# Kernel tuning notes

Hardware: AMD Instinct MI355X
Metric: run time of the kernel (lower is better)

## Reference

```python
import jax, jax.numpy as jnp
from jax import lax
import numpy as np

GAMMA = 0.25        # inv_temp
C_SCALE = 1.0       # spectral_scale
STRIDE = 8          # patch stride (== patch_size, non-overlapping)


def setup_inputs() -> dict:
    key = jax.random.key(0)
    ks = jax.random.split(key, 9)
    B, C, H = 1024, 3, 64
    D, NP, M, NH, R, P = 256, 64, 1024, 8, 32, 8
    return {
        "x": jax.random.normal(ks[0], (B, C, H, H), jnp.float32),
        "z": jax.random.normal(ks[1], (B, NP, D), jnp.float32),
        "encoder_weight": jax.random.normal(ks[2], (D, C, P, P), jnp.float32) * 0.05,
        "encoder_bias": jax.random.normal(ks[3], (D,), jnp.float32) * 0.05,
        "visible_bias": jax.random.normal(ks[4], (C, H, H), jnp.float32) * 0.05,
        "pos_bias": jax.random.normal(ks[5], (NP, D), jnp.float32) * 0.05,
        "memory_weight": jax.random.normal(ks[6], (D, M), jnp.float32) * 0.05,
        "W_Q": jax.random.normal(ks[7], (NH, R, D), jnp.float32) * 0.05,
        "W_K": jax.random.normal(ks[8], (NH, R, D), jnp.float32) * 0.05,
    }


def reference(x, z, encoder_weight, encoder_bias, visible_bias, pos_bias,
              memory_weight, W_Q, W_K):
    """E = 0.5||x||^2 + 0.5||z||^2 - Phi_coupling(x, z); returns (B,)."""
    B = x.shape[0]
    D = encoder_weight.shape[0]

    quad_x = 0.5 * jnp.sum(x * x, axis=(1, 2, 3))
    quad_z = 0.5 * jnp.sum(z * z, axis=(1, 2))

    # visible-bias coupling
    phi_vis = jnp.sum(visible_bias[None] * x, axis=(1, 2, 3))

    # conv encode: (B, D, gh, gw) -> (B, NP, D)
    enc = lax.conv_general_dilated(
        x, C_SCALE * encoder_weight, window_strides=(STRIDE, STRIDE),
        padding='VALID', dimension_numbers=('NCHW', 'OIHW', 'NCHW'))
    encoded = enc.reshape(B, D, -1).transpose(0, 2, 1)  # (B, NP, D)

    # enc_act = 'none' -> identity
    phi_enc = jnp.sum(encoded * z, axis=(1, 2))
    phi_bias = jnp.sum(z * encoder_bias, axis=(1, 2))
    phi_pos = jnp.sum(z * pos_bias[None], axis=(1, 2))

    # memory ReLU^2 term: (B, NP, M)
    mem_proj = jnp.einsum('bpd,dm->bpm', z, C_SCALE * memory_weight)
    phi_mem = jnp.sum(jnp.square(jax.nn.relu(mem_proj)), axis=(1, 2))

    # Hopfield attention logsumexp term
    Q = jnp.einsum('bpd,hrd->bhrp', z, C_SCALE * W_Q)  # (B, H, R, NP)
    K = jnp.einsum('bpd,hrd->bhrp', z, C_SCALE * W_K)
    A = jnp.einsum('bhdm,bhdn->bhmn', Q, K)            # (B, H, NP, NP)
    phi_att = jnp.sum(jax.scipy.special.logsumexp(GAMMA * A, axis=-1),
                      axis=(1, 2)) / GAMMA

    coupling = phi_vis + phi_enc + phi_bias + phi_pos + phi_mem + phi_att
    return quad_x + quad_z - coupling
```

## Files before the change

kernel.cpp:

```cpp
#include <hip/hip_runtime.h>
#include <hip/hip_bf16.h>

#define GAMMA 0.25f


typedef __attribute__((ext_vector_type(8))) short short8;
typedef __attribute__((ext_vector_type(4))) float f32x4;

__device__ __forceinline__ float dot4(float4 a, float4 b) {
  return fmaf(a.x, b.x, fmaf(a.y, b.y, fmaf(a.z, b.z, a.w * b.w)));
}

__device__ __forceinline__ void fma4(float4& a, float s, float4 w) {
  a.x = fmaf(s, w.x, a.x); a.y = fmaf(s, w.y, a.y);
  a.z = fmaf(s, w.z, a.z); a.w = fmaf(s, w.w, a.w);
}

__device__ __forceinline__ ushort f2bf(float f) {
  __hip_bfloat16 h = __float2bfloat16(f);
  return *reinterpret_cast<ushort*>(&h);
}

__device__ __forceinline__ float bf2f(ushort u) {
  union { unsigned int i; float f; } v;
  v.i = ((unsigned int)u) << 16;
  return v.f;
}

__device__ __forceinline__ float block_sum_256(float v, float* tmp) {
#pragma unroll
  for (int off = 32; off; off >>= 1) v += __shfl_down(v, off, 64);
  int w = threadIdx.x >> 6;
  if ((threadIdx.x & 63) == 0) tmp[w] = v;
  __syncthreads();
  return tmp[0] + tmp[1] + tmp[2] + tmp[3];
}

__global__ __launch_bounds__(256) void k_z_cvt2(const float* __restrict__ z,
                                                const float* __restrict__ eb,
                                                const float* __restrict__ pb,
                                                float* __restrict__ out,
                                                ushort* __restrict__ zb16) {
  __shared__ float tmp[4];
  int bid = blockIdx.x, b = bid >> 1, hz = bid & 1, t = threadIdx.x;
  const float4* zb = (const float4*)(z + (size_t)b * 16384);
  const float4* pb4 = (const float4*)pb;
  const float4* eb4 = (const float4*)eb;
  ushort4* z16o = (ushort4*)(zb16 + (size_t)b * 16384);
  float s = 0.f;
  const int i0 = hz * 2048;
  for (int i = i0 + t; i < i0 + 2048; i += 256) {
    float4 zv = zb[i];
    float4 pv = pb4[i];
    float4 ev = eb4[i & 63];
    float4 c;
    c.x = pv.x + ev.x; c.y = pv.y + ev.y; c.z = pv.z + ev.z; c.w = pv.w + ev.w;
    s += 0.5f * dot4(zv, zv) - dot4(zv, c);
    ushort4 o;
    o.x = f2bf(zv.x); o.y = f2bf(zv.y); o.z = f2bf(zv.z); o.w = f2bf(zv.w);
    z16o[i] = o;
  }
  float r = block_sum_256(s, tmp);
  if (t == 0) atomicAdd(out + b, r);
}

__global__ __launch_bounds__(256) void k_cvt_weights_v4(
    const float* __restrict__ wq, const float* __restrict__ wk,
    const float* __restrict__ ew, const float* __restrict__ mw,
    ushort* __restrict__ wcf, ushort* __restrict__ ewt,
    ushort* __restrict__ mtf) {
  int bid = blockIdx.x, t = threadIdx.x;
  ushort o[8];
  if (bid < 64) {
    int tid = bid * 256 + t;
    int frag = tid >> 6, l = tid & 63;
    int ctg = frag >> 3, kc = frag & 7;
    int col = ctg * 16 + (l & 15);
    int h = col >> 6, qk = (col >> 5) & 1, rr = col & 31;
    int k0 = kc * 32 + (l >> 4) * 8;
    const float* s = (qk ? wk : wq) + ((size_t)h * 32 + rr) * 256 + k0;
#pragma unroll
    for (int i = 0; i < 8; ++i) o[i] = f2bf(s[i]);
    *(ushort4*)(wcf + (size_t)tid * 8) = *(ushort4*)&o[0];
    *(ushort4*)(wcf + (size_t)tid * 8 + 4) = *(ushort4*)&o[4];
  } else if (bid < 88) {
    int tid = (bid - 64) * 256 + t;
    int frag = tid >> 6, l = tid & 63;
    int ks = frag / 12, ct = frag % 12;
    const float* s = ew + (size_t)(ks * 32 + (l >> 4) * 8) * 192 +
                     ct * 16 + (l & 15);
#pragma unroll
    for (int i = 0; i < 8; ++i) o[i] = f2bf(s[(size_t)i * 192]);
    *(ushort4*)(ewt + (size_t)tid * 8) = *(ushort4*)&o[0];
    *(ushort4*)(ewt + (size_t)tid * 8 + 4) = *(ushort4*)&o[4];
  } else {
    int tid = (bid - 88) * 256 + t;
    int frag = tid >> 6, l = tid & 63;
    int C = frag >> 3, kc = frag & 7;
    int k0 = kc * 32 + (l >> 4) * 8, col = C * 16 + (l & 15);
#pragma unroll
    for (int i = 0; i < 8; ++i) o[i] = f2bf(mw[(size_t)(k0 + i) * 1024 + col]);
    *(ushort4*)(mtf + (size_t)tid * 8) = *(ushort4*)&o[0];
    *(ushort4*)(mtf + (size_t)tid * 8 + 4) = *(ushort4*)&o[4];
  }
}

__global__ __launch_bounds__(256) void k_enc_v4(
    const float* __restrict__ x, const float* __restrict__ vb,
    const ushort* __restrict__ ewt, const ushort* __restrict__ zb16,
    float* __restrict__ out) {
  __shared__ ushort xs[12288];
  __shared__ ushort ebuf[2][6144];
  __shared__ float tmp[4];
  const int b = blockIdx.x, t = threadIdx.x, l = t & 63, w = t >> 6;
  const int q = l >> 4, m = l & 15;

  const ushort* Az = zb16 + ((size_t)b * 64 + 16 * w + m) * 256 + q * 8;
  short8 a[8];
#pragma unroll
  for (int ks = 0; ks < 8; ++ks) a[ks] = *(const short8*)(Az + ks * 32);

  short8 st[3];
#pragma unroll
  for (int i = 0; i < 3; ++i)
    st[i] = *(const short8*)(ewt + (size_t)(t + i * 256) * 8);

  const float4* xb = (const float4*)(x + (size_t)b * 12288);
  const float4* vb4 = (const float4*)vb;
  ushort4* xs4 = (ushort4*)xs;
  float s = 0.f;
  for (int i = t; i < 3072; i += 256) {
    float4 xv = xb[i];
    float4 bv = vb4[i];
    s += 0.5f * dot4(xv, xv) - dot4(bv, xv);
    ushort4 o;
    o.x = f2bf(xv.x); o.y = f2bf(xv.y); o.z = f2bf(xv.z); o.w = f2bf(xv.w);
    xs4[i] = o;
  }
#pragma unroll
  for (int i = 0; i < 3; ++i)
    *(short8*)(ebuf[0] + (size_t)(t + i * 256) * 8) = st[i];
  __syncthreads();

  f32x4 acc[12];
#pragma unroll
  for (int ct = 0; ct < 12; ++ct) acc[ct] = f32x4{0.f, 0.f, 0.f, 0.f};

#pragma unroll
  for (int ks = 0; ks < 8; ++ks) {
    const int cur = ks & 1;
    if (ks < 7) {
#pragma unroll
      for (int i = 0; i < 3; ++i)
        st[i] = *(const short8*)(ewt + (size_t)(ks + 1) * 6144 +
                                 (size_t)(t + i * 256) * 8);
    }
#pragma unroll
    for (int ct = 0; ct < 12; ++ct) {
      short8 bv = *(const short8*)(ebuf[cur] + (size_t)(ct * 64 + l) * 8);
      acc[ct] = __builtin_amdgcn_mfma_f32_16x16x32_bf16(a[ks], bv, acc[ct], 0, 0, 0);
    }
    if (ks < 7) {
#pragma unroll
      for (int i = 0; i < 3; ++i)
        *(short8*)(ebuf[cur ^ 1] + (size_t)(t + i * 256) * 8) = st[i];
    }
    __syncthreads();
  }

#pragma unroll
  for (int ct = 0; ct < 12; ++ct) {
#pragma unroll
    for (int reg = 0; reg < 4; ++reg) {
      const int p = 16 * w + 4 * q + reg, gi = p >> 3, gj = p & 7;
      const int k = ct * 16 + m, c = k >> 6, r2 = k & 63;
      const int ii = r2 >> 3, jj = r2 & 7;
      s -= acc[ct][reg] * bf2f(xs[c * 4096 + (gi * 8 + ii) * 64 + gj * 8 + jj]);
    }
  }
  float r = block_sum_256(s, tmp);
  if (t == 0) atomicAdd(out + b, r);
}

__global__ __launch_bounds__(256) void k_mem_v5(const ushort* __restrict__ zb,
                                                const ushort* __restrict__ mtf,
                                                float* __restrict__ out) {
  __shared__ ushort zf[2048 * 8];
  __shared__ float tmp[4];
  const int t = threadIdx.x, l = t & 63, w = t >> 6;
  const int b = blockIdx.x >> 1, cth = blockIdx.x & 1;

#pragma unroll
  for (int j = 0; j < 8; ++j) {
    int i = t + j * 256;
    int l2 = i & 63, ks = (i >> 6) & 7, w2 = i >> 9;
    short8 v = *(const short8*)(zb + ((size_t)b * 64 + 16 * w2 + (l2 & 15)) * 256
                                + ks * 32 + (l2 >> 4) * 8);
    *(short8*)(zf + (size_t)i * 8) = v;
  }
  __syncthreads();

  float s = 0.f;
#pragma unroll 1
  for (int ctl = 0; ctl < 2; ++ctl) {
    const int ct = cth * 2 + ctl;
    const ushort* Bb = mtf + ((size_t)(ct * 16 + w * 4) * 8) * 512 + (size_t)l * 8;
    short8 fb[2][4];
#pragma unroll
    for (int c = 0; c < 4; ++c) fb[0][c] = *(const short8*)(Bb + (c * 8 + 0) * 512);
#pragma unroll
    for (int c = 0; c < 4; ++c) fb[1][c] = *(const short8*)(Bb + (c * 8 + 1) * 512);

    f32x4 acc[4][4];
#pragma unroll
    for (int r = 0; r < 4; ++r)
#pragma unroll
      for (int c = 0; c < 4; ++c) acc[r][c] = f32x4{0.f, 0.f, 0.f, 0.f};

#pragma unroll
    for (int kc = 0; kc < 8; ++kc) {
      const int cur = kc & 1;
      short8 a4[4];
#pragma unroll
      for (int r = 0; r < 4; ++r)
        a4[r] = *(const short8*)(zf + (size_t)((r * 8 + kc) * 64 + l) * 8);
#pragma unroll
      for (int r = 0; r < 4; ++r)
#pragma unroll
        for (int c = 0; c < 4; ++c)
          acc[r][c] = __builtin_amdgcn_mfma_f32_16x16x32_bf16(a4[r], fb[cur][c],
                                                              acc[r][c], 0, 0, 0);
      if (kc < 6) {
#pragma unroll
        for (int c = 0; c < 4; ++c)
          fb[cur][c] = *(const short8*)(Bb + (c * 8 + kc + 2) * 512);
      }
    }
#pragma unroll
    for (int r = 0; r < 4; ++r)
#pragma unroll
      for (int c = 0; c < 4; ++c)
#pragma unroll
        for (int e = 0; e < 4; ++e) {
          float rr = fmaxf(acc[r][c][e], 0.f);
          s = fmaf(rr, rr, s);
        }
  }
  float r = block_sum_256(s, tmp);
  if (t == 0) atomicAdd(out + b, -r);
}

__global__ __launch_bounds__(256) void k_attn_v6(
    const ushort* __restrict__ zb, const ushort* __restrict__ wcf,
    float* __restrict__ out) {
  __shared__ ushort ubuf[64 * 264];
  __shared__ float tmp[4];
  const int t = threadIdx.x, l = t & 63, w = t >> 6;
  const int b = blockIdx.x >> 1, half = blockIdx.x & 1;
  const int q = l >> 4, m = l & 15;

#pragma unroll
  for (int j = 0; j < 8; ++j) {
    int i = t + j * 256;
    int l2 = i & 63, ks = (i >> 6) & 7, w2 = i >> 9;
    short8 v = *(const short8*)(zb + ((size_t)b * 64 + 16 * w2 + (l2 & 15)) * 256
                                + ks * 32 + (l2 >> 4) * 8);
    *(short8*)(ubuf + (size_t)i * 8) = v;
  }
  __syncthreads();

  const ushort* Bb = wcf + ((size_t)((half * 16 + w * 4) * 8)) * 512 +
                     (size_t)l * 8;
  short8 fb[2][4];
#pragma unroll
  for (int c = 0; c < 4; ++c) fb[0][c] = *(const short8*)(Bb + (c * 8 + 0) * 512);
#pragma unroll
  for (int c = 0; c < 4; ++c) fb[1][c] = *(const short8*)(Bb + (c * 8 + 1) * 512);

  f32x4 acc[4][4];
#pragma unroll
  for (int r = 0; r < 4; ++r)
#pragma unroll
    for (int c = 0; c < 4; ++c) acc[r][c] = f32x4{0.f, 0.f, 0.f, 0.f};

#pragma unroll
  for (int kc = 0; kc < 8; ++kc) {
    const int cur = kc & 1;
    short8 a4[4];
#pragma unroll
    for (int r = 0; r < 4; ++r)
      a4[r] = *(const short8*)(ubuf + (size_t)((r * 8 + kc) * 64 + l) * 8);
#pragma unroll
    for (int r = 0; r < 4; ++r)
#pragma unroll
      for (int c = 0; c < 4; ++c)
        acc[r][c] = __builtin_amdgcn_mfma_f32_16x16x32_bf16(a4[r], fb[cur][c],
                                                            acc[r][c], 0, 0, 0);
    if (kc < 6) {
#pragma unroll
      for (int c = 0; c < 4; ++c)
        fb[cur][c] = *(const short8*)(Bb + (c * 8 + kc + 2) * 512);
    }
  }
  __syncthreads();

  ushort* dstg = ubuf;
#pragma unroll
  for (int rt = 0; rt < 4; ++rt)
#pragma unroll
    for (int c = 0; c < 4; ++c)
#pragma unroll
      for (int reg = 0; reg < 4; ++reg)
        dstg[(size_t)(16 * rt + 4 * q + reg) * 264 + (4 * w + c) * 16 + m] =
            f2bf(acc[rt][c][reg]);
  __syncthreads();

  float part = 0.f;
#pragma unroll
  for (int hh = 0; hh < 4; ++hh) {
    short8 qa = *(const short8*)(dstg + (size_t)(16 * w + m) * 264 +
                                 hh * 64 + q * 8);
    f32x4 a2[4];
#pragma unroll
    for (int nt = 0; nt < 4; ++nt) {
      short8 kb = *(const short8*)(dstg + (size_t)(16 * nt + m) * 264 +
                                   hh * 64 + 32 + q * 8);
      a2[nt] = __builtin_amdgcn_mfma_f32_16x16x32_bf16(
          qa, kb, f32x4{0.f, 0.f, 0.f, 0.f}, 0, 0, 0);
    }
#pragma unroll
    for (int reg = 0; reg < 4; ++reg) {
      float e = __expf(GAMMA * a2[0][reg]) + __expf(GAMMA * a2[1][reg]) +
                __expf(GAMMA * a2[2][reg]) + __expf(GAMMA * a2[3][reg]);
      e += __shfl_xor(e, 1, 64);
      e += __shfl_xor(e, 2, 64);
      e += __shfl_xor(e, 4, 64);
      e += __shfl_xor(e, 8, 64);
      part += (m == 0) ? __logf(e) : 0.f;
    }
  }
  float tot = block_sum_256(part, tmp);
  if (t == 0) atomicAdd(out + b, -tot * (1.0f / GAMMA));
}

__global__ __launch_bounds__(256) void k_xz(const float* __restrict__ x,
                                            const float* __restrict__ z,
                                            const float* __restrict__ vb,
                                            const float* __restrict__ eb,
                                            const float* __restrict__ pb,
                                            float* __restrict__ out) {
  __shared__ float tmp[4];
  int b = blockIdx.x, t = threadIdx.x;
  const float4* xb = (const float4*)(x + (size_t)b * 12288);
  const float4* vb4 = (const float4*)vb;
  float s = 0.f;
  for (int i = t; i < 3072; i += 256) {
    float4 xv = xb[i];
    float4 bv = vb4[i];
    s += 0.5f * dot4(xv, xv) - dot4(bv, xv);
  }
  const float4* zb = (const float4*)(z + (size_t)b * 16384);
  const float4* pb4 = (const float4*)pb;
  const float4* eb4 = (const float4*)eb;
  for (int i = t; i < 4096; i += 256) {
    float4 zv = zb[i];
    float4 pv = pb4[i];
    float4 ev = eb4[i & 63];
    float4 c;
    c.x = pv.x + ev.x; c.y = pv.y + ev.y; c.z = pv.z + ev.z; c.w = pv.w + ev.w;
    s += 0.5f * dot4(zv, zv) - dot4(zv, c);
  }
  float r = block_sum_256(s, tmp);
  if (t == 0) out[b] = r;
}

__global__ __launch_bounds__(256) void k_enc(const float* __restrict__ x,
                                             const float* __restrict__ z,
                                             const float* __restrict__ ew,
                                             float* __restrict__ out) {
  __shared__ float xs[12288];
  __shared__ float tmp[4];
  int b = blockIdx.x, t = threadIdx.x;
  const float4* xb4 = (const float4*)(x + (size_t)b * 12288);
  for (int i = t; i < 3072; i += 256) ((float4*)xs)[i] = xb4[i];
  __syncthreads();

  float acc[64];
#pragma unroll
  for (int p = 0; p < 64; ++p) acc[p] = 0.f;

  for (int k4 = 0; k4 < 48; ++k4) {
    float4 wv = *(const float4*)(ew + (size_t)t * 192 + k4 * 4);
    int c = k4 >> 4;
    int ii = (k4 >> 1) & 7;
    int jh = (k4 & 1) * 4;
    const float* base = xs + c * 4096 + ii * 64 + jh;
#pragma unroll
    for (int p = 0; p < 64; ++p) {
      float4 pv = *(const float4*)(base + (p >> 3) * 512 + (p & 7) * 8);
      acc[p] = fmaf(wv.x, pv.x,
               fmaf(wv.y, pv.y, fmaf(wv.z, pv.z, fmaf(wv.w, pv.w, acc[p]))));
    }
  }
  const float* zb = z + (size_t)b * 16384;
  float s = 0.f;
#pragma unroll
  for (int p = 0; p < 64; ++p) s += acc[p] * zb[p * 256 + t];
  float r = block_sum_256(s, tmp);
  if (t == 0) atomicAdd(out + b, -r);
}

__global__ __launch_bounds__(256) void k_mem(const float* __restrict__ z,
                                             const float* __restrict__ mw,
                                             float* __restrict__ out) {
  __shared__ float zs[16 * 256];
  __shared__ float tmp[4];
  int b = blockIdx.x >> 2, pt = blockIdx.x & 3, t = threadIdx.x;
  const float4* zb4 = (const float4*)(z + (size_t)b * 16384 + pt * 4096);
  for (int i = t; i < 1024; i += 256) ((float4*)zs)[i] = zb4[i];
  __syncthreads();

  const float4* m4 = (const float4*)mw;
  float4 acc[16];
#pragma unroll
  for (int pp = 0; pp < 16; ++pp) acc[pp] = make_float4(0.f, 0.f, 0.f, 0.f);

#pragma unroll 2
  for (int k4 = 0; k4 < 64; ++k4) {
    float4 w0 = m4[(4 * k4 + 0) * 256 + t];
    float4 w1 = m4[(4 * k4 + 1) * 256 + t];
    float4 w2 = m4[(4 * k4 + 2) * 256 + t];
    float4 w3 = m4[(4 * k4 + 3) * 256 + t];
#pragma unroll
    for (int pp = 0; pp < 16; ++pp) {
      float4 zv = *(const float4*)&zs[pp * 256 + k4 * 4];
      fma4(acc[pp], zv.x, w0);
      fma4(acc[pp], zv.y, w1);
      fma4(acc[pp], zv.z, w2);
      fma4(acc[pp], zv.w, w3);
    }
  }
  float total = 0.f;
#pragma unroll
  for (int pp = 0; pp < 16; ++pp) {
    float r;
    r = fmaxf(acc[pp].x, 0.f); total = fmaf(r, r, total);
    r = fmaxf(acc[pp].y, 0.f); total = fmaf(r, r, total);
    r = fmaxf(acc[pp].z, 0.f); total = fmaf(r, r, total);
    r = fmaxf(acc[pp].w, 0.f); total = fmaf(r, r, total);
  }
  float r = block_sum_256(total, tmp);
  if (t == 0) atomicAdd(out + b, -r);
}

__global__ __launch_bounds__(256) void k_attn(const float* __restrict__ z,
                                              const float* __restrict__ wq,
                                              const float* __restrict__ wk,
                                              float* __restrict__ out) {
  __shared__ float lds[8192];
  __shared__ float red[4];
  const int b = blockIdx.x >> 1, half = blockIdx.x & 1;
  const int t = threadIdx.x;
  const int lane = t & 63;
  const int w = __builtin_amdgcn_readfirstlane(t >> 6);
  const float4* zb4 = (const float4*)(z + (size_t)b * 16384);

  float qa[4][8], ka[4][8];
#pragma unroll
  for (int hh = 0; hh < 4; ++hh)
#pragma unroll
    for (int j = 0; j < 8; ++j) { qa[hh][j] = 0.f; ka[hh][j] = 0.f; }

  float4* lds4 = (float4*)lds;
  for (int dc = 0; dc < 2; ++dc) {
    __syncthreads();
    for (int i = t; i < 2048; i += 256) {
      int p = i >> 5, ld4 = i & 31;
      lds4[ld4 * 64 + (p ^ (ld4 & 7))] = zb4[p * 64 + dc * 32 + ld4];
    }
    __syncthreads();
#pragma unroll
    for (int hh = 0; hh < 4; ++hh) {
      int h = half * 4 + hh;
      const float* Wqb = wq + (size_t)h * 8192 + (size_t)(w * 8) * 256 + dc * 128;
      const float* Wkb = wk + (size_t)h * 8192 + (size_t)(w * 8) * 256 + dc * 128;
      for (int ld4 = 0; ld4 < 32; ++ld4) {
        float4 wv[8], kv[8];
#pragma unroll
        for (int j = 0; j < 8; ++j) {
          wv[j] = *(const float4*)(Wqb + j * 256 + ld4 * 4);
          kv[j] = *(const float4*)(Wkb + j * 256 + ld4 * 4);
        }
        float4 zv = lds4[ld4 * 64 + (lane ^ (ld4 & 7))];
#pragma unroll
        for (int j = 0; j < 8; ++j) {
          qa[hh][j] = fmaf(wv[j].x, zv.x, fmaf(wv[j].y, zv.y,
                      fmaf(wv[j].z, zv.z, fmaf(wv[j].w, zv.w, qa[hh][j]))));
          ka[hh][j] = fmaf(kv[j].x, zv.x, fmaf(kv[j].y, zv.y,
                      fmaf(kv[j].z, zv.z, fmaf(kv[j].w, zv.w, ka[hh][j]))));
        }
      }
    }
  }

  float* Qs = lds;
  float* Ks = lds + 2048;
  float lse = 0.f;
#pragma unroll
  for (int hh = 0; hh < 4; ++hh) {
    __syncthreads();
#pragma unroll
    for (int j = 0; j < 8; ++j) {
      Qs[(w * 8 + j) * 64 + lane] = qa[hh][j];
      Ks[(w * 8 + j) * 64 + lane] = ka[hh][j];
    }
    __syncthreads();
    float av[16];
#pragma unroll
    for (int mm = 0; mm < 16; ++mm) av[mm] = 0.f;
    for (int rr = 0; rr < 32; ++rr) {
      float kv = Ks[rr * 64 + lane];
      const float* qrow = &Qs[rr * 64 + w * 16];
      float4 q0 = *(const float4*)(qrow + 0);
      float4 q1 = *(const float4*)(qrow + 4);
      float4 q2 = *(const float4*)(qrow + 8);
      float4 q3 = *(const float4*)(qrow + 12);
      av[0]  = fmaf(q0.x, kv, av[0]);  av[1]  = fmaf(q0.y, kv, av[1]);
      av[2]  = fmaf(q0.z, kv, av[2]);  av[3]  = fmaf(q0.w, kv, av[3]);
      av[4]  = fmaf(q1.x, kv, av[4]);  av[5]  = fmaf(q1.y, kv, av[5]);
      av[6]  = fmaf(q1.z, kv, av[6]);  av[7]  = fmaf(q1.w, kv, av[7]);
      av[8]  = fmaf(q2.x, kv, av[8]);  av[9]  = fmaf(q2.y, kv, av[9]);
      av[10] = fmaf(q2.z, kv, av[10]); av[11] = fmaf(q2.w, kv, av[11]);
      av[12] = fmaf(q3.x, kv, av[12]); av[13] = fmaf(q3.y, kv, av[13]);
      av[14] = fmaf(q3.z, kv, av[14]); av[15] = fmaf(q3.w, kv, av[15]);
    }
#pragma unroll
    for (int mm = 0; mm < 16; ++mm) {
      float e = __expf(GAMMA * av[mm]);
#pragma unroll
      for (int off = 32; off; off >>= 1) e += __shfl_xor(e, off, 64);
      lse += __logf(e);
    }
  }
  if (lane == 0) red[w] = lse;
  __syncthreads();
  if (t == 0)
    atomicAdd(out + b, -(red[0] + red[1] + red[2] + red[3]) * (1.0f / GAMMA));
}

extern "C" void kernel_launch(void* const* d_in, const int* in_sizes, int n_in,
                              void* d_out, int out_size, void* d_ws,
                              size_t ws_size, hipStream_t stream) {
  (void)in_sizes; (void)n_in; (void)out_size;
  const float* x  = (const float*)d_in[0];
  const float* z  = (const float*)d_in[1];
  const float* ew = (const float*)d_in[2];
  const float* eb = (const float*)d_in[3];
  const float* vb = (const float*)d_in[4];
  const float* pb = (const float*)d_in[5];
  const float* mw = (const float*)d_in[6];
  const float* wq = (const float*)d_in[7];
  const float* wk = (const float*)d_in[8];
  float* out = (float*)d_out;

  const size_t Z_B  = (size_t)1024 * 64 * 256 * 2;
  const size_t MT_B = (size_t)1024 * 256 * 2;
  const size_t EW_B = (size_t)96 * 64 * 8 * 2;
  const size_t WC_B = (size_t)512 * 256 * 2;
  const size_t FULL = Z_B + MT_B + EW_B + WC_B;

  ushort* zb16 = (ushort*)d_ws;
  ushort* mtf  = (ushort*)((char*)d_ws + Z_B);
  ushort* ewt  = (ushort*)((char*)d_ws + Z_B + MT_B);
  ushort* wcf  = (ushort*)((char*)d_ws + Z_B + MT_B + EW_B);

  if (ws_size >= FULL) {
    hipMemsetAsync(out, 0, 1024 * sizeof(float), stream);
    k_z_cvt2<<<2048, 256, 0, stream>>>(z, eb, pb, out, zb16);
    k_cvt_weights_v4<<<216, 256, 0, stream>>>(wq, wk, ew, mw, wcf, ewt, mtf);
    k_enc_v4 <<<1024, 256, 0, stream>>>(x, vb, ewt, zb16, out);
    k_mem_v5 <<<2048, 256, 0, stream>>>(zb16, mtf, out);
    k_attn_v6<<<2048, 256, 0, stream>>>(zb16, wcf, out);
  } else {
    k_xz  <<<1024, 256, 0, stream>>>(x, z, vb, eb, pb, out);
    k_enc <<<1024, 256, 0, stream>>>(x, z, ew, out);
    k_mem <<<4096, 256, 0, stream>>>(z, mw, out);
    k_attn<<<2048, 256, 0, stream>>>(z, wq, wk, out);
  }
}
```

Baseline: 253.9 us.

## Fuse z conversion, memory and attention terms into one per-batch kernel

Replaces the separate z-to-bf16 conversion, memory ReLU² and attention kernels with a single kernel per batch element. It loads fp32 z once, converts it into shared memory in MFMA fragment layout, then runs both GEMMs from LDS. The fused kernel writes the output directly, so the memset and the 32 MB bf16 z workspace round-trip are gone. The encoder kernel now converts z from fp32 itself. Each block does more serial work and uses more LDS, and the grid is 1024 blocks instead of 2048, which lowers parallelism. The XOR-swizzled staging buffer is meant to reduce bank conflicts.

```diff
diff --git a/kernel.cpp b/kernel.cpp
--- a/kernel.cpp
+++ b/kernel.cpp
@@ -34,34 +34,6 @@
   if ((threadIdx.x & 63) == 0) tmp[w] = v;
   __syncthreads();
   return tmp[0] + tmp[1] + tmp[2] + tmp[3];
-}
-
-__global__ __launch_bounds__(256) void k_z_cvt2(const float* __restrict__ z,
-                                                const float* __restrict__ eb,
-                                                const float* __restrict__ pb,
-                                                float* __restrict__ out,
-                                                ushort* __restrict__ zb16) {
-  __shared__ float tmp[4];
-  int bid = blockIdx.x, b = bid >> 1, hz = bid & 1, t = threadIdx.x;
-  const float4* zb = (const float4*)(z + (size_t)b * 16384);
-  const float4* pb4 = (const float4*)pb;
-  const float4* eb4 = (const float4*)eb;
-  ushort4* z16o = (ushort4*)(zb16 + (size_t)b * 16384);
-  float s = 0.f;
-  const int i0 = hz * 2048;
-  for (int i = i0 + t; i < i0 + 2048; i += 256) {
-    float4 zv = zb[i];
-    float4 pv = pb4[i];
-    float4 ev = eb4[i & 63];
-    float4 c;
-    c.x = pv.x + ev.x; c.y = pv.y + ev.y; c.z = pv.z + ev.z; c.w = pv.w + ev.w;
-    s += 0.5f * dot4(zv, zv) - dot4(zv, c);
-    ushort4 o;
-    o.x = f2bf(zv.x); o.y = f2bf(zv.y); o.z = f2bf(zv.z); o.w = f2bf(zv.w);
-    z16o[i] = o;
-  }
-  float r = block_sum_256(s, tmp);
-  if (t == 0) atomicAdd(out + b, r);
 }
 
 __global__ __launch_bounds__(256) void k_cvt_weights_v4(
@@ -105,9 +77,173 @@
   }
 }
 
-__global__ __launch_bounds__(256) void k_enc_v4(
+__global__ __launch_bounds__(256) void k_mega(
+    const float* __restrict__ z, const float* __restrict__ eb,
+    const float* __restrict__ pb, const ushort* __restrict__ mtf,
+    const ushort* __restrict__ wcf, float* __restrict__ out) {
+  __shared__ ushort SL[32768];
+  const int t = threadIdx.x, l = t & 63, w = t >> 6;
+  const int b = blockIdx.x;
+  const int q = l >> 4, m = l & 15;
+  float s = 0.f;
+
+  {
+    const float4* zb4 = (const float4*)(z + (size_t)b * 16384);
+    const float4* pb4 = (const float4*)pb;
+    const float4* eb4 = (const float4*)eb;
+#pragma unroll
+    for (int n = 0; n < 16; ++n) {
+      int i = t + n * 256;
+      float4 zv = zb4[i];
+      float4 pv = pb4[i];
+      float4 ev = eb4[i & 63];
+      float4 c;
+      c.x = pv.x + ev.x; c.y = pv.y + ev.y;
+      c.z = pv.z + ev.z; c.w = pv.w + ev.w;
+      s += 0.5f * dot4(zv, zv) - dot4(zv, c);
+      int p = i >> 6, d4 = i & 63;
+      int ks = d4 >> 3, sub = (d4 & 7) >> 1, e0 = (d4 & 1) * 4;
+      int li = (p & 15) + sub * 16;
+      ushort4 o;
+      o.x = f2bf(zv.x); o.y = f2bf(zv.y); o.z = f2bf(zv.z); o.w = f2bf(zv.w);
+      *(ushort4*)(SL + (size_t)(((p >> 4) * 8 + ks) * 64 + li) * 8 + e0) = o;
+    }
+  }
+  __syncthreads();
+
+#pragma unroll 1
+  for (int ctl = 0; ctl < 4; ++ctl) {
+    const ushort* Bb = mtf + ((size_t)(ctl * 16 + w * 4) * 8) * 512 +
+                       (size_t)l * 8;
+    short8 fb[2][4];
+#pragma unroll
+    for (int c = 0; c < 4; ++c) fb[0][c] = *(const short8*)(Bb + (c * 8 + 0) * 512);
+#pragma unroll
+    for (int c = 0; c < 4; ++c) fb[1][c] = *(const short8*)(Bb + (c * 8 + 1) * 512);
+
+    f32x4 acc[4][4];
+#pragma unroll
+    for (int r = 0; r < 4; ++r)
+#pragma unroll
+      for (int c = 0; c < 4; ++c) acc[r][c] = f32x4{0.f, 0.f, 0.f, 0.f};
+
+#pragma unroll
+    for (int kc = 0; kc < 8; ++kc) {
+      const int cur = kc & 1;
+      short8 a4[4];
+#pragma unroll
+      for (int r = 0; r < 4; ++r)
+        a4[r] = *(const short8*)(SL + (size_t)((r * 8 + kc) * 64 + l) * 8);
+#pragma unroll
+      for (int r = 0; r < 4; ++r)
+#pragma unroll
+        for (int c = 0; c < 4; ++c)
+          acc[r][c] = __builtin_amdgcn_mfma_f32_16x16x32_bf16(a4[r], fb[cur][c],
+                                                              acc[r][c], 0, 0, 0);
+      if (kc < 6) {
+#pragma unroll
+        for (int c = 0; c < 4; ++c)
+          fb[cur][c] = *(const short8*)(Bb + (c * 8 + kc + 2) * 512);
+      }
+    }
+#pragma unroll
+    for (int r = 0; r < 4; ++r)
+#pragma unroll
+      for (int c = 0; c < 4; ++c)
+#pragma unroll
+        for (int e = 0; e < 4; ++e) {
+          float rr = fmaxf(acc[r][c][e], 0.f);
+          s -= rr * rr;
+        }
+  }
+
+  float part = 0.f;
+  char* dstg = (char*)(SL + 16384);
+#pragma unroll 1
+  for (int half = 0; half < 2; ++half) {
+    const ushort* Bb = wcf + ((size_t)((half * 16 + w * 4) * 8)) * 512 +
+                       (size_t)l * 8;
+    short8 fb[2][4];
+#pragma unroll
+    for (int c = 0; c < 4; ++c) fb[0][c] = *(const short8*)(Bb + (c * 8 + 0) * 512);
+#pragma unroll
+    for (int c = 0; c < 4; ++c) fb[1][c] = *(const short8*)(Bb + (c * 8 + 1) * 512);
+
+    f32x4 acc[4][4];
+#pragma unroll
+    for (int r = 0; r < 4; ++r)
+#pragma unroll
+      for (int c = 0; c < 4; ++c) acc[r][c] = f32x4{0.f, 0.f, 0.f, 0.f};
+
+#pragma unroll
+    for (int kc = 0; kc < 8; ++kc) {
+      const int cur = kc & 1;
+      short8 a4[4];
+#pragma unroll
+      for (int r = 0; r < 4; ++r)
+        a4[r] = *(const short8*)(SL + (size_t)((r * 8 + kc) * 64 + l) * 8);
+#pragma unroll
+      for (int r = 0; r < 4; ++r)
+#pragma unroll
+        for (int c = 0; c < 4; ++c)
+          acc[r][c] = __builtin_amdgcn_mfma_f32_16x16x32_bf16(a4[r], fb[cur][c],
+                                                              acc[r][c], 0, 0, 0);
+      if (kc < 6) {
+#pragma unroll
+        for (int c = 0; c < 4; ++c)
+          fb[cur][c] = *(const short8*)(Bb + (c * 8 + kc + 2) * 512);
+      }
+    }
+
+#pragma unroll
+    for (int rt = 0; rt < 4; ++rt)
+#pragma unroll
+      for (int c = 0; c < 4; ++c)
+#pragma unroll
+        for (int reg = 0; reg < 4; ++reg) {
+          int row = 16 * rt + 4 * q + reg;
+          int col = (4 * w + c) * 16 + m;
+          int ba = ((row * 256 + col) * 2) ^ ((row & 7) << 4);
+          *(ushort*)(dstg + ba) = f2bf(acc[rt][c][reg]);
+        }
+    __syncthreads();
+
+#pragma unroll
+    for (int hh = 0; hh < 4; ++hh) {
+      int rowq = 16 * w + m;
+      short8 qa = *(const short8*)(
+          dstg + (((rowq * 256 + hh * 64 + q * 8) * 2) ^ ((rowq & 7) << 4)));
+      f32x4 a2[4];
+#pragma unroll
+      for (int nt = 0; nt < 4; ++nt) {
+        int rowk = 16 * nt + m;
+        short8 kb = *(const short8*)(
+            dstg + (((rowk * 256 + hh * 64 + 32 + q * 8) * 2) ^ ((rowk & 7) << 4)));
+        a2[nt] = __builtin_amdgcn_mfma_f32_16x16x32_bf16(
+            qa, kb, f32x4{0.f, 0.f, 0.f, 0.f}, 0, 0, 0);
+      }
+#pragma unroll
+      for (int reg = 0; reg < 4; ++reg) {
+        float e = __expf(GAMMA * a2[0][reg]) + __expf(GAMMA * a2[1][reg]) +
+                  __expf(GAMMA * a2[2][reg]) + __expf(GAMMA * a2[3][reg]);
+        e += __shfl_xor(e, 1, 64);
+        e += __shfl_xor(e, 2, 64);
+        e += __shfl_xor(e, 4, 64);
+        e += __shfl_xor(e, 8, 64);
+        part += (m == 0) ? __logf(e) : 0.f;
+      }
+    }
+    __syncthreads();
+  }
+  s -= part * (1.0f / GAMMA);
+
+  float r = block_sum_256(s, (float*)SL);
+  if (t == 0) out[b] = r;
+}
+
+__global__ __launch_bounds__(256) void k_enc_v5(
     const float* __restrict__ x, const float* __restrict__ vb,
-    const ushort* __restrict__ ewt, const ushort* __restrict__ zb16,
+    const float* __restrict__ z, const ushort* __restrict__ ewt,
     float* __restrict__ out) {
   __shared__ ushort xs[12288];
   __shared__ ushort ebuf[2][6144];
@@ -115,10 +251,17 @@
   const int b = blockIdx.x, t = threadIdx.x, l = t & 63, w = t >> 6;
   const int q = l >> 4, m = l & 15;
 
-  const ushort* Az = zb16 + ((size_t)b * 64 + 16 * w + m) * 256 + q * 8;
+  const float* Zr = z + (size_t)b * 16384 + (size_t)(16 * w + m) * 256 + q * 8;
   short8 a[8];
 #pragma unroll
-  for (int ks = 0; ks < 8; ++ks) a[ks] = *(const short8*)(Az + ks * 32);
+  for (int ks = 0; ks < 8; ++ks) {
+    float4 u = *(const float4*)(Zr + ks * 32);
+    float4 v = *(const float4*)(Zr + ks * 32 + 4);
+    ushort o[8];
+    o[0] = f2bf(u.x); o[1] = f2bf(u.y); o[2] = f2bf(u.z); o[3] = f2bf(u.w);
+    o[4] = f2bf(v.x); o[5] = f2bf(v.y); o[6] = f2bf(v.z); o[7] = f2bf(v.w);
+    a[ks] = *(short8*)o;
+  }
 
   short8 st[3];
 #pragma unroll
@@ -180,167 +323,6 @@
   }
   float r = block_sum_256(s, tmp);
   if (t == 0) atomicAdd(out + b, r);
-}
-
-__global__ __launch_bounds__(256) void k_mem_v5(const ushort* __restrict__ zb,
-                                                const ushort* __restrict__ mtf,
-                                                float* __restrict__ out) {
-  __shared__ ushort zf[2048 * 8];
-  __shared__ float tmp[4];
-  const int t = threadIdx.x, l = t & 63, w = t >> 6;
-  const int b = blockIdx.x >> 1, cth = blockIdx.x & 1;
-
-#pragma unroll
-  for (int j = 0; j < 8; ++j) {
-    int i = t + j * 256;
-    int l2 = i & 63, ks = (i >> 6) & 7, w2 = i >> 9;
-    short8 v = *(const short8*)(zb + ((size_t)b * 64 + 16 * w2 + (l2 & 15)) * 256
-                                + ks * 32 + (l2 >> 4) * 8);
-    *(short8*)(zf + (size_t)i * 8) = v;
-  }
-  __syncthreads();
-
-  float s = 0.f;
-#pragma unroll 1
-  for (int ctl = 0; ctl < 2; ++ctl) {
-    const int ct = cth * 2 + ctl;
-    const ushort* Bb = mtf + ((size_t)(ct * 16 + w * 4) * 8) * 512 + (size_t)l * 8;
-    short8 fb[2][4];
-#pragma unroll
-    for (int c = 0; c < 4; ++c) fb[0][c] = *(const short8*)(Bb + (c * 8 + 0) * 512);
-#pragma unroll
-    for (int c = 0; c < 4; ++c) fb[1][c] = *(const short8*)(Bb + (c * 8 + 1) * 512);
-
-    f32x4 acc[4][4];
-#pragma unroll
-    for (int r = 0; r < 4; ++r)
-#pragma unroll
-      for (int c = 0; c < 4; ++c) acc[r][c] = f32x4{0.f, 0.f, 0.f, 0.f};
-
-#pragma unroll
-    for (int kc = 0; kc < 8; ++kc) {
-      const int cur = kc & 1;
-      short8 a4[4];
-#pragma unroll
-      for (int r = 0; r < 4; ++r)
-        a4[r] = *(const short8*)(zf + (size_t)((r * 8 + kc) * 64 + l) * 8);
-#pragma unroll
-      for (int r = 0; r < 4; ++r)
-#pragma unroll
-        for (int c = 0; c < 4; ++c)
-          acc[r][c] = __builtin_amdgcn_mfma_f32_16x16x32_bf16(a4[r], fb[cur][c],
-                                                              acc[r][c], 0, 0, 0);
-      if (kc < 6) {
-#pragma unroll
-        for (int c = 0; c < 4; ++c)
-          fb[cur][c] = *(const short8*)(Bb + (c * 8 + kc + 2) * 512);
-      }
-    }
-#pragma unroll
-    for (int r = 0; r < 4; ++r)
-#pragma unroll
-      for (int c = 0; c < 4; ++c)
-#pragma unroll
-        for (int e = 0; e < 4; ++e) {
-          float rr = fmaxf(acc[r][c][e], 0.f);
-          s = fmaf(rr, rr, s);
-        }
-  }
-  float r = block_sum_256(s, tmp);
-  if (t == 0) atomicAdd(out + b, -r);
-}
-
-__global__ __launch_bounds__(256) void k_attn_v6(
-    const ushort* __restrict__ zb, const ushort* __restrict__ wcf,
-    float* __restrict__ out) {
-  __shared__ ushort ubuf[64 * 264];
-  __shared__ float tmp[4];
-  const int t = threadIdx.x, l = t & 63, w = t >> 6;
-  const int b = blockIdx.x >> 1, half = blockIdx.x & 1;
-  const int q = l >> 4, m = l & 15;
-
-#pragma unroll
-  for (int j = 0; j < 8; ++j) {
-    int i = t + j * 256;
-    int l2 = i & 63, ks = (i >> 6) & 7, w2 = i >> 9;
-    short8 v = *(const short8*)(zb + ((size_t)b * 64 + 16 * w2 + (l2 & 15)) * 256
-                                + ks * 32 + (l2 >> 4) * 8);
-    *(short8*)(ubuf + (size_t)i * 8) = v;
-  }
-  __syncthreads();
-
-  const ushort* Bb = wcf + ((size_t)((half * 16 + w * 4) * 8)) * 512 +
-                     (size_t)l * 8;
-  short8 fb[2][4];
-#pragma unroll
-  for (int c = 0; c < 4; ++c) fb[0][c] = *(const short8*)(Bb + (c * 8 + 0) * 512);
-#pragma unroll
-  for (int c = 0; c < 4; ++c) fb[1][c] = *(const short8*)(Bb + (c * 8 + 1) * 512);
-
-  f32x4 acc[4][4];
-#pragma unroll
-  for (int r = 0; r < 4; ++r)
-#pragma unroll
-    for (int c = 0; c < 4; ++c) acc[r][c] = f32x4{0.f, 0.f, 0.f, 0.f};
-
-#pragma unroll
-  for (int kc = 0; kc < 8; ++kc) {
-    const int cur = kc & 1;
-    short8 a4[4];
-#pragma unroll
-    for (int r = 0; r < 4; ++r)
-      a4[r] = *(const short8*)(ubuf + (size_t)((r * 8 + kc) * 64 + l) * 8);
-#pragma unroll
-    for (int r = 0; r < 4; ++r)
-#pragma unroll
-      for (int c = 0; c < 4; ++c)
-        acc[r][c] = __builtin_amdgcn_mfma_f32_16x16x32_bf16(a4[r], fb[cur][c],
-                                                            acc[r][c], 0, 0, 0);
-    if (kc < 6) {
-#pragma unroll
-      for (int c = 0; c < 4; ++c)
-        fb[cur][c] = *(const short8*)(Bb + (c * 8 + kc + 2) * 512);
-    }
-  }
-  __syncthreads();
-
-  ushort* dstg = ubuf;
-#pragma unroll
-  for (int rt = 0; rt < 4; ++rt)
-#pragma unroll
-    for (int c = 0; c < 4; ++c)
-#pragma unroll
-      for (int reg = 0; reg < 4; ++reg)
-        dstg[(size_t)(16 * rt + 4 * q + reg) * 264 + (4 * w + c) * 16 + m] =
-            f2bf(acc[rt][c][reg]);
-  __syncthreads();
-
-  float part = 0.f;
-#pragma unroll
-  for (int hh = 0; hh < 4; ++hh) {
-    short8 qa = *(const short8*)(dstg + (size_t)(16 * w + m) * 264 +
-                                 hh * 64 + q * 8);
-    f32x4 a2[4];
-#pragma unroll
-    for (int nt = 0; nt < 4; ++nt) {
-      short8 kb = *(const short8*)(dstg + (size_t)(16 * nt + m) * 264 +
-                                   hh * 64 + 32 + q * 8);
-      a2[nt] = __builtin_amdgcn_mfma_f32_16x16x32_bf16(
-          qa, kb, f32x4{0.f, 0.f, 0.f, 0.f}, 0, 0, 0);
-    }
-#pragma unroll
-    for (int reg = 0; reg < 4; ++reg) {
-      float e = __expf(GAMMA * a2[0][reg]) + __expf(GAMMA * a2[1][reg]) +
-                __expf(GAMMA * a2[2][reg]) + __expf(GAMMA * a2[3][reg]);
-      e += __shfl_xor(e, 1, 64);
-      e += __shfl_xor(e, 2, 64);
-      e += __shfl_xor(e, 4, 64);
-      e += __shfl_xor(e, 8, 64);
-      part += (m == 0) ? __logf(e) : 0.f;
-    }
-  }
-  float tot = block_sum_256(part, tmp);
-  if (t == 0) atomicAdd(out + b, -tot * (1.0f / GAMMA));
 }
 
 __global__ __launch_bounds__(256) void k_xz(const float* __restrict__ x,
@@ -563,24 +545,19 @@
   const float* wk = (const float*)d_in[8];
   float* out = (float*)d_out;
 
-  const size_t Z_B  = (size_t)1024 * 64 * 256 * 2;
   const size_t MT_B = (size_t)1024 * 256 * 2;
+  const size_t WC_B = (size_t)512 * 256 * 2;
   const size_t EW_B = (size_t)96 * 64 * 8 * 2;
-  const size_t WC_B = (size_t)512 * 256 * 2;
-  const size_t FULL = Z_B + MT_B + EW_B + WC_B;
-
-  ushort* zb16 = (ushort*)d_ws;
-  ushort* mtf  = (ushort*)((char*)d_ws + Z_B);
-  ushort* ewt  = (ushort*)((char*)d_ws + Z_B + MT_B);
-  ushort* wcf  = (ushort*)((char*)d_ws + Z_B + MT_B + EW_B);
+  const size_t FULL = MT_B + WC_B + EW_B;
+
+  ushort* mtf = (ushort*)d_ws;
+  ushort* wcf = (ushort*)((char*)d_ws + MT_B);
+  ushort* ewt = (ushort*)((char*)d_ws + MT_B + WC_B);
 
   if (ws_size >= FULL) {
-    hipMemsetAsync(out, 0, 1024 * sizeof(float), stream);
-    k_z_cvt2<<<2048, 256, 0, stream>>>(z, eb, pb, out, zb16);
     k_cvt_weights_v4<<<216, 256, 0, stream>>>(wq, wk, ew, mw, wcf, ewt, mtf);
-    k_enc_v4 <<<1024, 256, 0, stream>>>(x, vb, ewt, zb16, out);
-    k_mem_v5 <<<2048, 256, 0, stream>>>(zb16, mtf, out);
-    k_attn_v6<<<2048, 256, 0, stream>>>(zb16, wcf, out);
+    k_mega  <<<1024, 256, 0, stream>>>(z, eb, pb, mtf, wcf, out);
+    k_enc_v5<<<1024, 256, 0, stream>>>(x, vb, z, ewt, out);
   } else {
     k_xz  <<<1024, 256, 0, stream>>>(x, z, vb, eb, pb, out);
     k_enc <<<1024, 256, 0, stream>>>(x, z, ew, out);
```

Result: faster. 222.4 us (-12.4%).
